# Kernel optimization log

Hardware: AMD Instinct MI355X
Metric: run time of the kernel (lower is better)

Reference implementation:

```python
import jax, jax.numpy as jnp
import numpy as np

T = 4                 # number of spiking timesteps (module init T)
NUM_THRESHOLDS = 8    # K thresholds: thresh / 2**k
B, C, H, W = 32, 128, 32, 32


def setup_inputs() -> dict:
    key = jax.random.key(0)
    x = jax.random.normal(key, ((T + 1) * B, C, H, W), dtype=jnp.float32)
    thresh = jnp.ones((1,), dtype=jnp.float32)
    return {"x": x, "thresh": thresh}


def _forward(x, thresh):
    # ExpandTemporalDim(T+1): [(T+1)*B, C, H, W] -> [T+1, B, C, H, W]
    xt_all = x.reshape((T + 1, B, C, H, W))
    # thre_shaped: [K, 1, 1, 1, 1]
    time_steps = (2.0 ** jnp.arange(NUM_THRESHOLDS, dtype=jnp.float32)).reshape(
        (NUM_THRESHOLDS, 1, 1, 1, 1))
    thre = thresh / time_steps
    thre_thr = thre * 0.75
    bias = xt_all[0]

    def step(carry, inp):
        mem, cum, exp_in, exp_out = carry
        xt, t = inp
        mem = mem + xt - bias + exp_in - exp_out
        cum = cum + exp_out
        # [K, B, C, H, W] indicator tensors
        pos = (mem[None] >= thre_thr).astype(jnp.float32)
        neg = ((mem[None] <= -thre_thr).astype(jnp.float32)
               * (cum[None] >= thre).astype(jnp.float32))
        # pos_true[0] = pos[0]; pos_true[k] = pos[k] - pos[k-1]
        zk = jnp.zeros_like(pos[:1])
        pos_true = jnp.diff(pos, axis=0, prepend=zk)
        neg_true = jnp.diff(neg, axis=0, prepend=zk)
        spike = (jnp.sum(thre * pos_true, axis=0)
                 - jnp.sum(thre * neg_true, axis=0))
        mem = mem - spike
        cum = cum + spike
        denom = t + 1.0
        exp_in = exp_in + (xt - bias) / denom
        exp_out = exp_out + spike / denom
        return (mem, cum, exp_in, exp_out), spike

    z = jnp.zeros_like(bias)
    carry0 = (z, z, bias, z)  # mem=0, cumulative_out=0, exp_in=x[0], exp_out=0
    ts = jnp.arange(T, dtype=jnp.float32)
    _, spikes = jax.lax.scan(step, carry0, (xt_all[1:], ts))
    # spike_pot[0] is zeros, then the T spikes; MergeTemporalDim flattens back
    out = jnp.concatenate([z[None], spikes], axis=0)
    return out.reshape(((T + 1) * B, C, H, W))


def reference(x, thresh):
    return _forward(x, thresh)
```

## Files before the change

### kernel.cpp

```cpp
#include <hip/hip_runtime.h>


constexpr int T_STEPS = 4;
constexpr int K_THR   = 8;

typedef float f32x4 __attribute__((ext_vector_type(4)));

__device__ __forceinline__ float div3_cr(float v) {
    const float c = 1.0f / 3.0f;
    float q = v * c;
    float r = __builtin_fmaf(-3.0f, q, v);
    return __builtin_fmaf(r, c, q);
}

__device__ __forceinline__ float spike_fast(float m, float c) {
    const unsigned B075 = 0x3F400000u;
    const unsigned B100 = 0x3F800000u;
    const float TT7 = 0.0058593750f;
    const float TH7 = 0.0078125f;

    const unsigned mb = (unsigned)__float_as_int(m);

    int dp = (int)(B075 - mb);
    int kp = (dp + 0x7FFFFF) >> 23;
    kp = kp < 0 ? 0 : kp;
    const float spv = __int_as_float((127 - kp) << 23);
    const float sp  = (m >= TT7) ? spv : 0.0f;

    int da = (int)(B075 - (mb & 0x7FFFFFFFu));
    int ka = (da + 0x7FFFFF) >> 23;
    ka = ka < 0 ? 0 : ka;
    int db = (int)(B100 - (unsigned)__float_as_int(c));
    int kb = (db + 0x7FFFFF) >> 23;
    kb = kb < 0 ? 0 : kb;
    const int kn = ka > kb ? ka : kb;
    const float snv = __int_as_float((127 - kn) << 23);
    const float sn  = (m <= -TT7 && c >= TH7) ? snv : 0.0f;

    return sp - sn;
}

__device__ __forceinline__ float spike_general(float m, float c, float th) {
    float sp = 0.f, sn = 0.f;
    #pragma unroll
    for (int k = K_THR - 1; k >= 0; --k) {
        const float thre = th * (1.0f / (float)(1 << k));
        const float tt   = 0.75f * thre;
        sp = (m >= tt) ? thre : sp;
        sn = (m <= -tt && c >= thre) ? thre : sn;
    }
    return sp - sn;
}

template <bool FAST>
__device__ __forceinline__ void run_body(const f32x4* __restrict__ xv,
                                         f32x4* __restrict__ ov,
                                         float th, int n4, int i)
{
    const f32x4 b4 = xv[i];
    const f32x4 x1 = xv[(size_t)1 * n4 + i];
    const f32x4 x2 = xv[(size_t)2 * n4 + i];
    const f32x4 x3 = xv[(size_t)3 * n4 + i];
    const f32x4 x4 = xv[(size_t)4 * n4 + i];

    f32x4 s1, s2, s3, s4;

    #pragma unroll
    for (int j = 0; j < 4; ++j) {
        const float b  = b4[j];
        float mem = 0.f, cum = 0.f, ein = b, eout = 0.f;

        {
            const float xt = x1[j];
            float m = (((mem + xt) - b) + ein) - eout;
            float c = cum + eout;
            const float spike = FAST ? spike_fast(m, c) : spike_general(m, c, th);
            m -= spike; c += spike;
            ein  += (xt - b);
            eout += spike;
            mem = m; cum = c; s1[j] = spike;
        }
        {
            const float xt = x2[j];
            float m = (((mem + xt) - b) + ein) - eout;
            float c = cum + eout;
            const float spike = FAST ? spike_fast(m, c) : spike_general(m, c, th);
            m -= spike; c += spike;
            ein  += (xt - b) * 0.5f;
            eout += spike * 0.5f;
            mem = m; cum = c; s2[j] = spike;
        }
        {
            const float xt = x3[j];
            float m = (((mem + xt) - b) + ein) - eout;
            float c = cum + eout;
            const float spike = FAST ? spike_fast(m, c) : spike_general(m, c, th);
            m -= spike; c += spike;
            ein  += div3_cr(xt - b);
            eout += FAST ? (spike * (1.0f / 3.0f)) : div3_cr(spike);
            mem = m; cum = c; s3[j] = spike;
        }
        {
            const float xt = x4[j];
            float m = (((mem + xt) - b) + ein) - eout;
            float c = cum + eout;
            const float spike = FAST ? spike_fast(m, c) : spike_general(m, c, th);
            s4[j] = spike;
        }
    }

    __builtin_nontemporal_store((f32x4){0.f, 0.f, 0.f, 0.f}, &ov[i]);
    __builtin_nontemporal_store(s1, &ov[(size_t)1 * n4 + i]);
    __builtin_nontemporal_store(s2, &ov[(size_t)2 * n4 + i]);
    __builtin_nontemporal_store(s3, &ov[(size_t)3 * n4 + i]);
    __builtin_nontemporal_store(s4, &ov[(size_t)4 * n4 + i]);
}

__global__ __launch_bounds__(256) void mth_kernel(
    const float* __restrict__ x, const float* __restrict__ thresh,
    float* __restrict__ out, int n4)
{
    const float th = __uint_as_float(
        __builtin_amdgcn_readfirstlane(__float_as_uint(thresh[0])));

    const int i = blockIdx.x * 256 + threadIdx.x;
    if (i >= n4) return;

    const f32x4* __restrict__ xv = reinterpret_cast<const f32x4*>(x);
    f32x4* __restrict__ ov       = reinterpret_cast<f32x4*>(out);

    if (th == 1.0f) run_body<true >(xv, ov, th, n4, i);
    else            run_body<false>(xv, ov, th, n4, i);
}

extern "C" void kernel_launch(void* const* d_in, const int* in_sizes, int n_in,
                              void* d_out, int out_size, void* d_ws, size_t ws_size,
                              hipStream_t stream)
{
    const float* x      = (const float*)d_in[0];
    const float* thresh = (const float*)d_in[1];
    float* out          = (float*)d_out;

    const int N  = in_sizes[0] / (T_STEPS + 1);
    const int n4 = N / 4;
    const int block = 256;
    const int grid  = (n4 + block - 1) / block;

    mth_kernel<<<grid, block, 0, stream>>>(x, thresh, out, n4);
}
```

Baseline: 156.0 us.

## Switch to grid-stride loop with software prefetch of next chunk

Replaces the one-chunk-per-thread launch with a fixed grid of 1024 blocks that loop in grid-stride fashion. Each iteration issues the loads for the next chunk before computing the current one, so memory latency overlaps with compute. Nontemporal stores are also replaced with ordinary stores. The cost is fewer resident waves to hide latency and extra registers for the prefetched data, and ordinary stores may pollute the cache.

```diff
diff --git a/kernel.cpp b/kernel.cpp
--- a/kernel.cpp
+++ b/kernel.cpp
@@ -53,31 +53,22 @@
 }
 
 template <bool FAST>
-__device__ __forceinline__ void run_body(const f32x4* __restrict__ xv,
-                                         f32x4* __restrict__ ov,
-                                         float th, int n4, int i)
+__device__ __forceinline__ void compute_chunk(
+    const f32x4& b4, const f32x4& x1, const f32x4& x2,
+    const f32x4& x3, const f32x4& x4, float th,
+    f32x4& s1, f32x4& s2, f32x4& s3, f32x4& s4)
 {
-    const f32x4 b4 = xv[i];
-    const f32x4 x1 = xv[(size_t)1 * n4 + i];
-    const f32x4 x2 = xv[(size_t)2 * n4 + i];
-    const f32x4 x3 = xv[(size_t)3 * n4 + i];
-    const f32x4 x4 = xv[(size_t)4 * n4 + i];
-
-    f32x4 s1, s2, s3, s4;
-
     #pragma unroll
     for (int j = 0; j < 4; ++j) {
-        const float b  = b4[j];
+        const float b = b4[j];
         float mem = 0.f, cum = 0.f, ein = b, eout = 0.f;
-
         {
             const float xt = x1[j];
             float m = (((mem + xt) - b) + ein) - eout;
             float c = cum + eout;
             const float spike = FAST ? spike_fast(m, c) : spike_general(m, c, th);
             m -= spike; c += spike;
-            ein  += (xt - b);
-            eout += spike;
+            ein += (xt - b); eout += spike;
             mem = m; cum = c; s1[j] = spike;
         }
         {
@@ -86,8 +77,7 @@
             float c = cum + eout;
             const float spike = FAST ? spike_fast(m, c) : spike_general(m, c, th);
             m -= spike; c += spike;
-            ein  += (xt - b) * 0.5f;
-            eout += spike * 0.5f;
+            ein += (xt - b) * 0.5f; eout += spike * 0.5f;
             mem = m; cum = c; s2[j] = spike;
         }
         {
@@ -96,7 +86,7 @@
             float c = cum + eout;
             const float spike = FAST ? spike_fast(m, c) : spike_general(m, c, th);
             m -= spike; c += spike;
-            ein  += div3_cr(xt - b);
+            ein += div3_cr(xt - b);
             eout += FAST ? (spike * (1.0f / 3.0f)) : div3_cr(spike);
             mem = m; cum = c; s3[j] = spike;
         }
@@ -104,16 +94,48 @@
             const float xt = x4[j];
             float m = (((mem + xt) - b) + ein) - eout;
             float c = cum + eout;
-            const float spike = FAST ? spike_fast(m, c) : spike_general(m, c, th);
-            s4[j] = spike;
+            s4[j] = FAST ? spike_fast(m, c) : spike_general(m, c, th);
         }
     }
+}
 
-    __builtin_nontemporal_store((f32x4){0.f, 0.f, 0.f, 0.f}, &ov[i]);
-    __builtin_nontemporal_store(s1, &ov[(size_t)1 * n4 + i]);
-    __builtin_nontemporal_store(s2, &ov[(size_t)2 * n4 + i]);
-    __builtin_nontemporal_store(s3, &ov[(size_t)3 * n4 + i]);
-    __builtin_nontemporal_store(s4, &ov[(size_t)4 * n4 + i]);
+template <bool FAST>
+__device__ __forceinline__ void run_loop(const f32x4* __restrict__ xv,
+                                         f32x4* __restrict__ ov,
+                                         float th, int n4, int i, int stride)
+{
+    f32x4 b4 = xv[i];
+    f32x4 x1 = xv[(size_t)1 * n4 + i];
+    f32x4 x2 = xv[(size_t)2 * n4 + i];
+    f32x4 x3 = xv[(size_t)3 * n4 + i];
+    f32x4 x4 = xv[(size_t)4 * n4 + i];
+
+    for (;;) {
+        const int inext = i + stride;
+        const bool more = inext < n4;
+
+        f32x4 nb, n1, n2, n3, n4v;
+        if (more) {
+            nb  = xv[inext];
+            n1  = xv[(size_t)1 * n4 + inext];
+            n2  = xv[(size_t)2 * n4 + inext];
+            n3  = xv[(size_t)3 * n4 + inext];
+            n4v = xv[(size_t)4 * n4 + inext];
+        }
+
+        f32x4 s1, s2, s3, s4;
+        compute_chunk<FAST>(b4, x1, x2, x3, x4, th, s1, s2, s3, s4);
+
+        ov[i]                    = (f32x4){0.f, 0.f, 0.f, 0.f};
+        ov[(size_t)1 * n4 + i]   = s1;
+        ov[(size_t)2 * n4 + i]   = s2;
+        ov[(size_t)3 * n4 + i]   = s3;
+        ov[(size_t)4 * n4 + i]   = s4;
+
+        if (!more) break;
+        b4 = nb; x1 = n1; x2 = n2; x3 = n3; x4 = n4v;
+        i = inext;
+    }
 }
 
 __global__ __launch_bounds__(256) void mth_kernel(
@@ -123,14 +145,15 @@
     const float th = __uint_as_float(
         __builtin_amdgcn_readfirstlane(__float_as_uint(thresh[0])));
 
+    const int stride = gridDim.x * 256;
     const int i = blockIdx.x * 256 + threadIdx.x;
     if (i >= n4) return;
 
     const f32x4* __restrict__ xv = reinterpret_cast<const f32x4*>(x);
     f32x4* __restrict__ ov       = reinterpret_cast<f32x4*>(out);
 
-    if (th == 1.0f) run_body<true >(xv, ov, th, n4, i);
-    else            run_body<false>(xv, ov, th, n4, i);
+    if (th == 1.0f) run_loop<true >(xv, ov, th, n4, i, stride);
+    else            run_loop<false>(xv, ov, th, n4, i, stride);
 }
 
 extern "C" void kernel_launch(void* const* d_in, const int* in_sizes, int n_in,
@@ -143,8 +166,8 @@
 
     const int N  = in_sizes[0] / (T_STEPS + 1);
     const int n4 = N / 4;
+
     const int block = 256;
-    const int grid  = (n4 + block - 1) / block;
-
+    const int grid  = 1024;
     mth_kernel<<<grid, block, 0, stream>>>(x, thresh, out, n4);
 }
```

Measured after the change: 157.6 us. About the same (+1.0%).
